# Kernel tuning notes

Measured on AMD Instinct MI355X. Metric: run time of the kernel, lower is better.

## Reference

```python
import jax, jax.numpy as jnp
import numpy as np
from jax import lax

B, C, H, W = 4, 256, 128, 128
NH = 8
HD = C // NH  # 32
K = 7         # toodd(7) -> 7
DIL = 2
NBH = K // 2  # neighborhood radius


def _window_start(i, L, k, d):
    nh = k // 2
    if d <= 1:
        return max(i - nh, 0) + (L - i - nh - 1 if i + nh >= L else 0)
    ni = i - nh * d
    if ni < 0:
        return i % d
    if i + nh * d >= L:
        imodd = i % d
        a = (L // d) * d
        b = L - a
        if imodd < b:
            return L - b + imodd - 2 * nh * d
        return a + imodd - k * d
    return ni


def _pb_start(i, L, k, d):
    nh = k // 2
    if d <= 1:
        return nh + (nh - i if i < nh else 0) + (L - i - 1 - nh if i + nh >= L else 0)
    if i - nh * d < 0:
        return k - 1 - (i // d)
    if i + nh * d >= L:
        return (L - i - 1) // d
    return nh


# [L, K] neighbor indices per axis, and [L] relative-position-bias start offsets
IDX_H = np.array([[_window_start(i, H, K, DIL) + ki * DIL for ki in range(K)] for i in range(H)], dtype=np.int32)
IDX_W = np.array([[_window_start(j, W, K, DIL) + kj * DIL for kj in range(K)] for j in range(W)], dtype=np.int32)
PB_H = np.array([_pb_start(i, H, K, DIL) for i in range(H)], dtype=np.int32)
PB_W = np.array([_pb_start(j, W, K, DIL) for j in range(W)], dtype=np.int32)


def setup_inputs() -> dict:
    key = jax.random.key(0)
    ks = jax.random.split(key, 8)
    gain = 2.0 ** (-2.5)
    x = jax.random.normal(ks[0], (B, C, H, W), jnp.float32)
    # rotary tables in [-1, 1]
    sin = jax.random.uniform(ks[1], (H, W, HD), jnp.float32, minval=-1.0, maxval=1.0)
    cos = jax.random.uniform(ks[2], (H, W, HD), jnp.float32, minval=-1.0, maxval=1.0)
    w_qkv = jax.random.normal(ks[3], (3 * C, C), jnp.float32) * gain * (2.0 / (4 * C)) ** 0.5
    b_qkv = jnp.zeros((3 * C,), jnp.float32)
    w_lepe = jax.random.normal(ks[4], (C, 1, 5, 5), jnp.float32) * 0.02
    b_lepe = jnp.zeros((C,), jnp.float32)
    w_proj = jax.random.normal(ks[5], (C, C), jnp.float32) * gain * (1.0 / C) ** 0.5
    b_proj = jnp.zeros((C,), jnp.float32)
    rpb = jax.random.normal(ks[6], (NH, 2 * K - 1, 2 * K - 1), jnp.float32) * 0.02
    return {"x": x, "sin": sin, "cos": cos, "w_qkv": w_qkv, "b_qkv": b_qkv,
            "w_lepe": w_lepe, "b_lepe": b_lepe, "w_proj": w_proj, "b_proj": b_proj, "rpb": rpb}


def _rotate_every_two(t):
    t1 = t[..., ::2]
    t2 = t[..., 1::2]
    return jnp.stack([-t2, t1], axis=-1).reshape(t.shape)


def _forward(x, sin, cos, w_qkv, b_qkv, w_lepe, b_lepe, w_proj, b_proj, rpb):
    Bx, Cx, Hx, Wx = x.shape
    # 1x1 qkv conv
    qkv = jnp.einsum('oc,bchw->bohw', w_qkv, x) + b_qkv[None, :, None, None]
    v_chan = qkv[:, 2 * Cx:]
    # LePE: depthwise 5x5 conv on v channels
    lepe = lax.conv_general_dilated(v_chan, w_lepe, (1, 1), [(2, 2), (2, 2)],
                                    feature_group_count=Cx,
                                    dimension_numbers=('NCHW', 'OIHW', 'NCHW'))
    lepe = lepe + b_lepe[None, :, None, None]

    def split_heads(t):  # [B, n*c, H, W] -> [B, n, H, W, c]
        return t.reshape(Bx, NH, HD, Hx, Wx).transpose(0, 1, 3, 4, 2)

    q = split_heads(qkv[:, :Cx])
    k = split_heads(qkv[:, Cx:2 * Cx])
    v = split_heads(v_chan)

    q = (q * cos + _rotate_every_two(q) * sin) * (HD ** -0.5)
    k = k * cos + _rotate_every_two(k) * sin

    idx_h = jnp.asarray(IDX_H)
    idx_w = jnp.asarray(IDX_W)
    pb_h = jnp.asarray(PB_H)
    pb_w = jnp.asarray(PB_W)

    # na2d_qk: dilated neighborhood scores + relative position bias
    attn_slices = []
    for ki in range(K):
        kh = jnp.take(k, idx_h[:, ki], axis=2)          # [B,n,H,W,c]
        for kj in range(K):
            khw = jnp.take(kh, idx_w[:, kj], axis=3)    # [B,n,H,W,c]
            s = jnp.einsum('bnhwc,bnhwc->bnhw', q, khw)
            bias = rpb[:, pb_h + ki][:, :, pb_w + kj]    # [n,H,W]
            attn_slices.append(s + bias[None])
    attn = jnp.stack(attn_slices, axis=-1)               # [B,n,H,W,K*K]
    attn = jax.nn.softmax(attn, axis=-1)

    # na2d_av
    out = jnp.zeros_like(v)
    idx = 0
    for ki in range(K):
        vh = jnp.take(v, idx_h[:, ki], axis=2)
        for kj in range(K):
            vhw = jnp.take(vh, idx_w[:, kj], axis=3)
            out = out + attn[..., idx, None] * vhw
            idx += 1

    out = out.transpose(0, 1, 4, 2, 3).reshape(Bx, Cx, Hx, Wx)  # merge heads
    out = out + lepe
    return jnp.einsum('oc,bchw->bohw', w_proj, out) + b_proj[None, :, None, None]


def reference(x, sin, cos, w_qkv, b_qkv, w_lepe, b_lepe, w_proj, b_proj, rpb):
    return _forward(x, sin, cos, w_qkv, b_qkv, w_lepe, b_lepe, w_proj, b_proj, rpb)
```

## Files before the change

kernel.cpp:

```cpp
#include <hip/hip_runtime.h>
#include <cstddef>

#define HW 16384
#define WID 128

typedef __attribute__((ext_vector_type(8))) short short8;
typedef __attribute__((ext_vector_type(4))) float f32x4;

__device__ __forceinline__ int wstart(int i) {
    if (i < 6) return i & 1;
    if (i >= 122) return 114 + (i & 1);
    return i - 6;
}
__device__ __forceinline__ int pbstart(int i) {
    if (i < 6) return 6 - (i >> 1);
    if (i >= 122) return (127 - i) >> 1;
    return 3;
}

__device__ __forceinline__ unsigned short bf16rne(float f) {
    unsigned u = __builtin_bit_cast(unsigned, f);
    u += 0x7FFFu + ((u >> 16) & 1u);
    return (unsigned short)(u >> 16);
}
__device__ __forceinline__ void bsplit(float f, unsigned short& h, unsigned short& l) {
    h = bf16rne(f);
    float hf = __builtin_bit_cast(float, ((unsigned)h) << 16);
    l = bf16rne(f - hf);
}

__global__ __launch_bounds__(256) void pack_t(const float* __restrict__ src, size_t bstr,
                                              unsigned short* __restrict__ dh,
                                              unsigned short* __restrict__ dl) {
    __shared__ float sm[32][260];
    const int p0 = blockIdx.x * 256, c32 = blockIdx.y, b = blockIdx.z;
    const float* s = src + (size_t)b * bstr + (size_t)(c32 * 32) * HW + p0;
    const int t = threadIdx.x;
    const int rr = t >> 3, f = t & 7;
#pragma unroll
    for (int u = 0; u < 8; u++) {
        float4 v = *(const float4*)(s + (size_t)rr * HW + (f + 8 * u) * 4);
        *(float4*)&sm[rr][(f + 8 * u) * 4] = v;
    }
    __syncthreads();
    size_t off = ((size_t)(b * 8 + c32) * HW + p0 + t) * 32;
#pragma unroll
    for (int w = 0; w < 4; w++) {
        short8 vh, vl;
#pragma unroll
        for (int e = 0; e < 8; e++) {
            unsigned short h, lo_;
            bsplit(sm[w * 8 + e][t], h, lo_);
            vh[e] = (short)h;
            vl[e] = (short)lo_;
        }
        *(short8*)&dh[off + w * 8] = vh;
        *(short8*)&dl[off + w * 8] = vl;
    }
}

template <bool QKV>
__global__ __launch_bounds__(256, 2) void gemm_mfma(
    const float* __restrict__ Wm, const unsigned short* __restrict__ xh,
    const unsigned short* __restrict__ xl, const float* __restrict__ bias,
    const float* __restrict__ sinp, const float* __restrict__ cosp,
    float* __restrict__ Y, int NMT, int MT) {
    __shared__ unsigned short As_h[128][40], As_l[128][40];
    __shared__ unsigned short Bs_h[128][40], Bs_l[128][40];
    const int bid = blockIdx.x;
    const int xcd = bid & 7, r = bid >> 3;
    const int mt = r % NMT;
    const int q2 = r / NMT;
    const int nt = xcd * 16 + (q2 & 15);
    const int b = q2 >> 4;
    const int t = threadIdx.x;
    const int lane = t & 63, wid = t >> 6;
    const int wm = wid >> 1, wn = wid & 1;
    const int m0 = mt * 128;

    f32x4 acc[4][4];
#pragma unroll
    for (int i = 0; i < 4; i++)
#pragma unroll
        for (int j = 0; j < 4; j++) acc[i][j] = (f32x4){0.f, 0.f, 0.f, 0.f};

    const int sr = t >> 1, sh = t & 1;
    const float* arow = Wm + (size_t)(m0 + sr) * 256 + sh * 16;
    const unsigned short* bh_b = xh + ((size_t)(b * 8) * HW + (size_t)nt * 128 + sr) * 32 + sh * 16;
    const unsigned short* bl_b = xl + ((size_t)(b * 8) * HW + (size_t)nt * 128 + sr) * 32 + sh * 16;

    for (int ks = 0; ks < 8; ks++) {
        {
            const float* ap = arow + ks * 32;
#pragma unroll
            for (int g = 0; g < 2; g++) {
                float4 f0 = *(const float4*)(ap + g * 8);
                float4 f1 = *(const float4*)(ap + g * 8 + 4);
                float ff[8] = {f0.x, f0.y, f0.z, f0.w, f1.x, f1.y, f1.z, f1.w};
                short8 vh, vl;
#pragma unroll
                for (int e = 0; e < 8; e++) {
                    unsigned short h, lo_;
                    bsplit(ff[e], h, lo_);
                    vh[e] = (short)h;
                    vl[e] = (short)lo_;
                }
                *(short8*)&As_h[sr][sh * 16 + g * 8] = vh;
                *(short8*)&As_l[sr][sh * 16 + g * 8] = vl;
            }
        }
        {
            const unsigned short* bp = bh_b + (size_t)ks * HW * 32;
            const unsigned short* lp = bl_b + (size_t)ks * HW * 32;
            *(short8*)&Bs_h[sr][sh * 16] = *(const short8*)(bp);
            *(short8*)&Bs_h[sr][sh * 16 + 8] = *(const short8*)(bp + 8);
            *(short8*)&Bs_l[sr][sh * 16] = *(const short8*)(lp);
            *(short8*)&Bs_l[sr][sh * 16 + 8] = *(const short8*)(lp + 8);
        }
        __syncthreads();
        const int k8 = (lane >> 4) * 8;
        short8 a_h[4], a_l[4];
#pragma unroll
        for (int mi = 0; mi < 4; mi++) {
            int am = wm * 64 + mi * 16 + (lane & 15);
            a_h[mi] = *(const short8*)&As_h[am][k8];
            a_l[mi] = *(const short8*)&As_l[am][k8];
        }
#pragma unroll
        for (int ni = 0; ni < 4; ni++) {
            int bn = wn * 64 + ni * 16 + (lane & 15);
            short8 b_h = *(const short8*)&Bs_h[bn][k8];
            short8 b_l = *(const short8*)&Bs_l[bn][k8];
#pragma unroll
            for (int mi = 0; mi < 4; mi++) {
                acc[mi][ni] = __builtin_amdgcn_mfma_f32_16x16x32_bf16(a_h[mi], b_h, acc[mi][ni], 0, 0, 0);
                acc[mi][ni] = __builtin_amdgcn_mfma_f32_16x16x32_bf16(a_h[mi], b_l, acc[mi][ni], 0, 0, 0);
                acc[mi][ni] = __builtin_amdgcn_mfma_f32_16x16x32_bf16(a_l[mi], b_h, acc[mi][ni], 0, 0, 0);
            }
        }
        __syncthreads();
    }

    const int col = lane & 15, rq = (lane >> 4) * 4;
    const int s = QKV ? (mt >> 1) : 3;
#pragma unroll
    for (int mi = 0; mi < 4; mi++) {
        int mrow = m0 + wm * 64 + mi * 16 + rq;
        float b0 = bias[mrow], b1 = bias[mrow + 1], b2 = bias[mrow + 2], b3 = bias[mrow + 3];
#pragma unroll
        for (int ni = 0; ni < 4; ni++) {
            int p = nt * 128 + wn * 64 + ni * 16 + col;
            float v0 = acc[mi][ni][0] + b0, v1 = acc[mi][ni][1] + b1;
            float v2 = acc[mi][ni][2] + b2, v3 = acc[mi][ni][3] + b3;
            if (QKV && s < 2) {
                int d0 = (mi & 1) * 16 + rq;
                const float* cp = cosp + (size_t)p * 32 + d0;
                const float* sp = sinp + (size_t)p * 32 + d0;
                float c0 = cp[0], c1 = cp[1], c2 = cp[2], c3 = cp[3];
                float s0 = sp[0], s1 = sp[1], s2 = sp[2], s3 = sp[3];
                float n0 = v0 * c0 - v1 * s0, n1 = v1 * c1 + v0 * s1;
                float n2 = v2 * c2 - v3 * s2, n3 = v3 * c3 + v2 * s3;
                if (s == 0) {
                    const float sc = 0.17677669529663687f;
                    n0 *= sc; n1 *= sc; n2 *= sc; n3 *= sc;
                }
                v0 = n0; v1 = n1; v2 = n2; v3 = n3;
            }
            float* yp = Y + ((size_t)b * MT + mrow) * HW + p;
            yp[0] = v0;
            yp[HW] = v1;
            yp[2 * HW] = v2;
            yp[3 * HW] = v3;
        }
    }
}

__global__ __launch_bounds__(256) void attn_k(const float* __restrict__ qkv,
                                              const float* __restrict__ rpb,
                                              const float* __restrict__ wl,
                                              const float* __restrict__ bl,
                                              float* __restrict__ out) {
    __shared__ float sm[14 * 128];
    const int t = threadIdx.x;
    const int ty = t >> 7;
    const int j = t & 127;
    const int i0 = blockIdx.x * 2;
    const int i = i0 + ty;
    const int n = blockIdx.y, b = blockIdx.z;
    const int r0 = wstart(i0);

    const float* qb = qkv + ((size_t)b * 768 + n * 32) * HW;
    const float* kb = qb + (size_t)256 * HW;
    const float* vb = qb + (size_t)512 * HW;
    const int p = i * WID + j;

    const int ws_ = wstart(j);
    const int ph = pbstart(i), pw = pbstart(j);

    float sc[49];
    const float* rp = rpb + n * 169;
#pragma unroll
    for (int ki = 0; ki < 7; ki++)
#pragma unroll
        for (int kj = 0; kj < 7; kj++)
            sc[ki * 7 + kj] = rp[(ph + ki) * 13 + (pw + kj)];

    const float* smb = sm + ty * 128 + ws_;

    for (int c = 0; c < 32; c++) {
        __syncthreads();
        {
            const float* plane = kb + (size_t)c * HW + r0 * WID;
#pragma unroll
            for (int u = 0; u < 7; u++) sm[t + u * 256] = plane[t + u * 256];
        }
        __syncthreads();
        float qc = qb[(size_t)c * HW + p];
#pragma unroll
        for (int ki = 0; ki < 7; ki++) {
            const float* kib = smb + ki * 256;
#pragma unroll
            for (int kj = 0; kj < 7; kj++)
                sc[ki * 7 + kj] = fmaf(qc, kib[kj * 2], sc[ki * 7 + kj]);
        }
    }

    float mx = sc[0];
#pragma unroll
    for (int u = 1; u < 49; u++) mx = fmaxf(mx, sc[u]);
    float sum = 0.0f;
#pragma unroll
    for (int u = 0; u < 49; u++) {
        sc[u] = __expf(sc[u] - mx);
        sum += sc[u];
    }
    float inv = 1.0f / sum;
#pragma unroll
    for (int u = 0; u < 49; u++) sc[u] *= inv;

    float* ob = out + ((size_t)b * 768 + n * 32) * HW + p;
    const float* wbase = wl + (size_t)(n * 32) * 25;
    const float* blb = bl + n * 32;
    for (int c = 0; c < 32; c++) {
        __syncthreads();
        {
            const float* plane = vb + (size_t)c * HW + r0 * WID;
#pragma unroll
            for (int u = 0; u < 7; u++) sm[t + u * 256] = plane[t + u * 256];
        }
        __syncthreads();
        float oc = 0.0f;
#pragma unroll
        for (int ki = 0; ki < 7; ki++) {
            const float* kib = smb + ki * 256;
#pragma unroll
            for (int kj = 0; kj < 7; kj++)
                oc = fmaf(sc[ki * 7 + kj], kib[kj * 2], oc);
        }
        const float* wrow = wbase + c * 25;
        float lac = blb[c];
#pragma unroll
        for (int di = 0; di < 5; di++) {
            int ii = i + di - 2;
            if ((unsigned)ii < 128u) {
                const float* srow = sm + (ii - r0) * 128;
                const float* wr = wrow + di * 5;
#pragma unroll
                for (int dj = 0; dj < 5; dj++) {
                    int jj = j + dj - 2;
                    if ((unsigned)jj < 128u)
                        lac = fmaf(wr[dj], srow[jj], lac);
                }
            }
        }
        ob[(size_t)c * HW] = oc + lac;
    }
}

extern "C" void kernel_launch(void* const* d_in, const int* in_sizes, int n_in,
                              void* d_out, int out_size, void* d_ws, size_t ws_size,
                              hipStream_t stream) {
    const float* x = (const float*)d_in[0];
    const float* sinp = (const float*)d_in[1];
    const float* cosp = (const float*)d_in[2];
    const float* w_qkv = (const float*)d_in[3];
    const float* b_qkv = (const float*)d_in[4];
    const float* w_lepe = (const float*)d_in[5];
    const float* b_lepe = (const float*)d_in[6];
    const float* w_proj = (const float*)d_in[7];
    const float* b_proj = (const float*)d_in[8];
    const float* rpb = (const float*)d_in[9];
    float* out = (float*)d_out;

    unsigned short* xph = (unsigned short*)d_ws;
    unsigned short* xpl = xph + 16777216ull;
    float* qkvb = (float*)(xph + 33554432ull);

    pack_t<<<dim3(64, 8, 4), 256, 0, stream>>>(x, (size_t)256 * HW, xph, xpl);
    gemm_mfma<true><<<dim3(3072), 256, 0, stream>>>(w_qkv, xph, xpl, b_qkv, sinp, cosp,
                                                    qkvb, 6, 768);
    attn_k<<<dim3(64, 8, 4), 256, 0, stream>>>(qkvb, rpb, w_lepe, b_lepe, qkvb);
    pack_t<<<dim3(64, 8, 4), 256, 0, stream>>>(qkvb, (size_t)768 * HW, xph, xpl);
    gemm_mfma<false><<<dim3(1024), 256, 0, stream>>>(w_proj, xph, xpl, b_proj, nullptr, nullptr,
                                                     out, 2, 256);
}
```

Measured before the change: 440.0 us.

## Prefetch K/V planes into registers and enlarge attention blocks to four rows

The attention kernel now processes four output rows per 512-thread block instead of two, loading a 16-row shared window per channel, which cuts redundant halo reloads. The next channel's K/V plane and q value are prefetched into registers while the current channel is computed, hiding global load latency behind the neighborhood FMAs. The grid is also flattened and remapped so that adjacent row tiles of the same batch and head land on the same XCD, for better L2 locality. The costs are higher register pressure from the prefetch buffers and larger blocks, which may lower occupancy.

```diff
diff --git a/kernel.cpp b/kernel.cpp
--- a/kernel.cpp
+++ b/kernel.cpp
@@ -175,18 +175,22 @@
     }
 }
 
-__global__ __launch_bounds__(256) void attn_k(const float* __restrict__ qkv,
+__global__ __launch_bounds__(512) void attn_k(const float* __restrict__ qkv,
                                               const float* __restrict__ rpb,
                                               const float* __restrict__ wl,
                                               const float* __restrict__ bl,
                                               float* __restrict__ out) {
-    __shared__ float sm[14 * 128];
+    __shared__ float sm[16 * 128];
     const int t = threadIdx.x;
     const int ty = t >> 7;
     const int j = t & 127;
-    const int i0 = blockIdx.x * 2;
+    const int bid = blockIdx.x;
+    const int xcd = bid & 7, rr = bid >> 3;
+    const int it = xcd * 4 + (rr & 3);
+    const int nb = rr >> 2;
+    const int n = nb & 7, b = nb >> 3;
+    const int i0 = it * 4;
     const int i = i0 + ty;
-    const int n = blockIdx.y, b = blockIdx.z;
     const int r0 = wstart(i0);
 
     const float* qb = qkv + ((size_t)b * 768 + n * 32) * HW;
@@ -194,8 +198,16 @@
     const float* vb = qb + (size_t)512 * HW;
     const int p = i * WID + j;
 
-    const int ws_ = wstart(j);
+    const int hs = wstart(i), ws_ = wstart(j);
     const int ph = pbstart(i), pw = pbstart(j);
+
+    int gofs[4];
+#pragma unroll
+    for (int s = 0; s < 4; s++) {
+        int g = r0 + ty + 4 * s;
+        if (g > 127) g = 127;
+        gofs[s] = g * WID + j;
+    }
 
     float sc[49];
     const float* rp = rpb + n * 169;
@@ -205,17 +217,24 @@
         for (int kj = 0; kj < 7; kj++)
             sc[ki * 7 + kj] = rp[(ph + ki) * 13 + (pw + kj)];
 
-    const float* smb = sm + ty * 128 + ws_;
-
+    const float* smb = sm + (hs - r0) * WID + ws_;
+
+    float rg[4], qn;
+#pragma unroll
+    for (int s = 0; s < 4; s++) rg[s] = kb[gofs[s]];
+    qn = qb[p];
     for (int c = 0; c < 32; c++) {
         __syncthreads();
-        {
-            const float* plane = kb + (size_t)c * HW + r0 * WID;
-#pragma unroll
-            for (int u = 0; u < 7; u++) sm[t + u * 256] = plane[t + u * 256];
-        }
-        __syncthreads();
-        float qc = qb[(size_t)c * HW + p];
+#pragma unroll
+        for (int s = 0; s < 4; s++) sm[(ty + 4 * s) * WID + j] = rg[s];
+        float qc = qn;
+        if (c < 31) {
+            const float* pl = kb + (size_t)(c + 1) * HW;
+#pragma unroll
+            for (int s = 0; s < 4; s++) rg[s] = pl[gofs[s]];
+            qn = qb[(size_t)(c + 1) * HW + p];
+        }
+        __syncthreads();
 #pragma unroll
         for (int ki = 0; ki < 7; ki++) {
             const float* kib = smb + ki * 256;
@@ -224,6 +243,9 @@
                 sc[ki * 7 + kj] = fmaf(qc, kib[kj * 2], sc[ki * 7 + kj]);
         }
     }
+
+#pragma unroll
+    for (int s = 0; s < 4; s++) rg[s] = vb[gofs[s]];
 
     float mx = sc[0];
 #pragma unroll
@@ -243,10 +265,12 @@
     const float* blb = bl + n * 32;
     for (int c = 0; c < 32; c++) {
         __syncthreads();
-        {
-            const float* plane = vb + (size_t)c * HW + r0 * WID;
-#pragma unroll
-            for (int u = 0; u < 7; u++) sm[t + u * 256] = plane[t + u * 256];
+#pragma unroll
+        for (int s = 0; s < 4; s++) sm[(ty + 4 * s) * WID + j] = rg[s];
+        if (c < 31) {
+            const float* pl = vb + (size_t)(c + 1) * HW;
+#pragma unroll
+            for (int s = 0; s < 4; s++) rg[s] = pl[gofs[s]];
         }
         __syncthreads();
         float oc = 0.0f;
@@ -263,7 +287,7 @@
         for (int di = 0; di < 5; di++) {
             int ii = i + di - 2;
             if ((unsigned)ii < 128u) {
-                const float* srow = sm + (ii - r0) * 128;
+                const float* srow = sm + (ii - r0) * WID;
                 const float* wr = wrow + di * 5;
 #pragma unroll
                 for (int dj = 0; dj < 5; dj++) {
@@ -299,7 +323,7 @@
     pack_t<<<dim3(64, 8, 4), 256, 0, stream>>>(x, (size_t)256 * HW, xph, xpl);
     gemm_mfma<true><<<dim3(3072), 256, 0, stream>>>(w_qkv, xph, xpl, b_qkv, sinp, cosp,
                                                     qkvb, 6, 768);
-    attn_k<<<dim3(64, 8, 4), 256, 0, stream>>>(qkvb, rpb, w_lepe, b_lepe, qkvb);
+    attn_k<<<dim3(1024), 512, 0, stream>>>(qkvb, rpb, w_lepe, b_lepe, qkvb);
     pack_t<<<dim3(64, 8, 4), 256, 0, stream>>>(qkvb, (size_t)768 * HW, xph, xpl);
     gemm_mfma<false><<<dim3(1024), 256, 0, stream>>>(w_proj, xph, xpl, b_proj, nullptr, nullptr,
                                                      out, 2, 256);
```

New measurement: 522.1 us. 18.7% more time.

## Retile attention kernel into 4x64 tiles with double-buffered two-channel LDS staging

Applied to the files above, without the earlier changes.

The neighborhood-attention kernel now works on 4-row by 64-column pixel tiles. Each tile stages an 18x88 halo window for two channels at a time into double-buffered shared memory, and the loads go through registers so the next channel pair is prefetched while the current one is computed. This halves the number of barriers, and block IDs are remapped so that row tiles are grouped per XCD for cache locality. The cost is higher register pressure (11 prefetch registers plus 49 scores) and some redundant halo loads at tile edges.

```diff
diff --git a/kernel.cpp b/kernel.cpp
--- a/kernel.cpp
+++ b/kernel.cpp
@@ -175,27 +175,52 @@
     }
 }
 
+#define SW 88
+#define CB 1408
+#define BUF 2816
 __global__ __launch_bounds__(256) void attn_k(const float* __restrict__ qkv,
                                               const float* __restrict__ rpb,
                                               const float* __restrict__ wl,
                                               const float* __restrict__ bl,
                                               float* __restrict__ out) {
-    __shared__ float sm[14 * 128];
+    __shared__ float sm[2 * BUF];
     const int t = threadIdx.x;
-    const int ty = t >> 7;
-    const int j = t & 127;
-    const int i0 = blockIdx.x * 2;
+    const int ty = t >> 6;
+    const int lj = t & 63;
+    const int bid = blockIdx.x;
+    const int xcd = bid & 7, rr = bid >> 3;
+    const int itc = rr & 3;
+    const int jt = (rr >> 2) & 1;
+    const int nb = rr >> 3;
+    const int n = nb & 7, b = nb >> 3;
+    const int it = xcd * 4 + itc;
+    const int i0 = it * 4;
+    const int j0 = jt * 64;
     const int i = i0 + ty;
-    const int n = blockIdx.y, b = blockIdx.z;
+    const int gj = j0 + lj;
     const int r0 = wstart(i0);
+    const int wc0 = wstart(j0);
 
     const float* qb = qkv + ((size_t)b * 768 + n * 32) * HW;
     const float* kb = qb + (size_t)256 * HW;
     const float* vb = qb + (size_t)512 * HW;
-    const int p = i * WID + j;
-
-    const int ws_ = wstart(j);
-    const int ph = pbstart(i), pw = pbstart(j);
+    const int p = i * WID + gj;
+
+    const int hs = wstart(i), ws_ = wstart(gj);
+    const int ph = pbstart(i), pw = pbstart(gj);
+
+    int goff[11];
+#pragma unroll
+    for (int u = 0; u < 11; u++) {
+        int d = u * 256 + t;
+        int sel = d >= CB;
+        int ld = d - sel * CB;
+        int r = ld / SW;
+        int cc = ld - r * SW;
+        int grow = r0 + r; if (grow > 127) grow = 127;
+        int gcol = wc0 + cc; if (gcol > 127) gcol = 127;
+        goff[u] = sel * HW + grow * WID + gcol;
+    }
 
     float sc[49];
     const float* rp = rpb + n * 169;
@@ -205,24 +230,44 @@
         for (int kj = 0; kj < 7; kj++)
             sc[ki * 7 + kj] = rp[(ph + ki) * 13 + (pw + kj)];
 
-    const float* smb = sm + ty * 128 + ws_;
-
-    for (int c = 0; c < 32; c++) {
+    const int abase = (hs - r0) * SW + (ws_ - wc0);
+    const int lrow0 = i - 2 - r0;
+    const int lcol0 = gj - 2 - wc0;
+
+    float rg[11];
+#pragma unroll
+    for (int u = 0; u < 11; u++) rg[u] = kb[goff[u]];
+    float qnA = qb[p], qnB = qb[HW + p];
+#pragma unroll
+    for (int u = 0; u < 11; u++) sm[u * 256 + t] = rg[u];
+    __syncthreads();
+
+    for (int cp = 0; cp < 16; cp++) {
+        const int cur = cp & 1;
+        const float* npl = (cp < 15) ? kb + (size_t)(cp + 1) * 2 * HW : vb;
+#pragma unroll
+        for (int u = 0; u < 11; u++) rg[u] = npl[goff[u]];
+        float qA = qnA, qB = qnB;
+        if (cp < 15) {
+            qnA = qb[(size_t)(2 * cp + 2) * HW + p];
+            qnB = qb[(size_t)(2 * cp + 3) * HW + p];
+        }
+        const float* s0 = sm + cur * BUF + abase;
+        const float* s1 = s0 + CB;
+#pragma unroll
+        for (int ki = 0; ki < 7; ki++) {
+            const float* a0 = s0 + ki * (2 * SW);
+            const float* a1 = s1 + ki * (2 * SW);
+#pragma unroll
+            for (int kj = 0; kj < 7; kj++) {
+                sc[ki * 7 + kj] = fmaf(qA, a0[kj * 2], sc[ki * 7 + kj]);
+                sc[ki * 7 + kj] = fmaf(qB, a1[kj * 2], sc[ki * 7 + kj]);
+            }
+        }
+        float* dst = sm + (cur ^ 1) * BUF;
+#pragma unroll
+        for (int u = 0; u < 11; u++) dst[u * 256 + t] = rg[u];
         __syncthreads();
-        {
-            const float* plane = kb + (size_t)c * HW + r0 * WID;
-#pragma unroll
-            for (int u = 0; u < 7; u++) sm[t + u * 256] = plane[t + u * 256];
-        }
-        __syncthreads();
-        float qc = qb[(size_t)c * HW + p];
-#pragma unroll
-        for (int ki = 0; ki < 7; ki++) {
-            const float* kib = smb + ki * 256;
-#pragma unroll
-            for (int kj = 0; kj < 7; kj++)
-                sc[ki * 7 + kj] = fmaf(qc, kib[kj * 2], sc[ki * 7 + kj]);
-        }
     }
 
     float mx = sc[0];
@@ -241,39 +286,50 @@
     float* ob = out + ((size_t)b * 768 + n * 32) * HW + p;
     const float* wbase = wl + (size_t)(n * 32) * 25;
     const float* blb = bl + n * 32;
-    for (int c = 0; c < 32; c++) {
+    for (int cp = 0; cp < 16; cp++) {
+        const int cur = cp & 1;
+        if (cp < 15) {
+            const float* npl = vb + (size_t)(cp + 1) * 2 * HW;
+#pragma unroll
+            for (int u = 0; u < 11; u++) rg[u] = npl[goff[u]];
+        }
+#pragma unroll
+        for (int ch = 0; ch < 2; ch++) {
+            const int cc = 2 * cp + ch;
+            const float* sv = sm + cur * BUF + ch * CB;
+            const float* sa = sv + abase;
+            float oc = 0.0f;
+#pragma unroll
+            for (int ki = 0; ki < 7; ki++) {
+                const float* a0 = sa + ki * (2 * SW);
+#pragma unroll
+                for (int kj = 0; kj < 7; kj++)
+                    oc = fmaf(sc[ki * 7 + kj], a0[kj * 2], oc);
+            }
+            const float* wrow = wbase + cc * 25;
+            float lac = blb[cc];
+#pragma unroll
+            for (int di = 0; di < 5; di++) {
+                int ii = i + di - 2;
+                if ((unsigned)ii < 128u) {
+                    const float* srow = sv + (lrow0 + di) * SW + lcol0;
+                    const float* wr = wrow + di * 5;
+#pragma unroll
+                    for (int dj = 0; dj < 5; dj++) {
+                        int jj = gj + dj - 2;
+                        if ((unsigned)jj < 128u)
+                            lac = fmaf(wr[dj], srow[dj], lac);
+                    }
+                }
+            }
+            ob[(size_t)cc * HW] = oc + lac;
+        }
+        if (cp < 15) {
+            float* dst = sm + (cur ^ 1) * BUF;
+#pragma unroll
+            for (int u = 0; u < 11; u++) dst[u * 256 + t] = rg[u];
+        }
         __syncthreads();
-        {
-            const float* plane = vb + (size_t)c * HW + r0 * WID;
-#pragma unroll
-            for (int u = 0; u < 7; u++) sm[t + u * 256] = plane[t + u * 256];
-        }
-        __syncthreads();
-        float oc = 0.0f;
-#pragma unroll
-        for (int ki = 0; ki < 7; ki++) {
-            const float* kib = smb + ki * 256;
-#pragma unroll
-            for (int kj = 0; kj < 7; kj++)
-                oc = fmaf(sc[ki * 7 + kj], kib[kj * 2], oc);
-        }
-        const float* wrow = wbase + c * 25;
-        float lac = blb[c];
-#pragma unroll
-        for (int di = 0; di < 5; di++) {
-            int ii = i + di - 2;
-            if ((unsigned)ii < 128u) {
-                const float* srow = sm + (ii - r0) * 128;
-                const float* wr = wrow + di * 5;
-#pragma unroll
-                for (int dj = 0; dj < 5; dj++) {
-                    int jj = j + dj - 2;
-                    if ((unsigned)jj < 128u)
-                        lac = fmaf(wr[dj], srow[jj], lac);
-                }
-            }
-        }
-        ob[(size_t)c * HW] = oc + lac;
     }
 }
 
@@ -299,7 +355,7 @@
     pack_t<<<dim3(64, 8, 4), 256, 0, stream>>>(x, (size_t)256 * HW, xph, xpl);
     gemm_mfma<true><<<dim3(3072), 256, 0, stream>>>(w_qkv, xph, xpl, b_qkv, sinp, cosp,
                                                     qkvb, 6, 768);
-    attn_k<<<dim3(64, 8, 4), 256, 0, stream>>>(qkvb, rpb, w_lepe, b_lepe, qkvb);
+    attn_k<<<dim3(2048), 256, 0, stream>>>(qkvb, rpb, w_lepe, b_lepe, qkvb);
     pack_t<<<dim3(64, 8, 4), 256, 0, stream>>>(qkvb, (size_t)768 * HW, xph, xpl);
     gemm_mfma<false><<<dim3(1024), 256, 0, stream>>>(w_proj, xph, xpl, b_proj, nullptr, nullptr,
                                                      out, 2, 256);
```

Result: slower. 464.8 us (+5.6%).

## Double-buffer K/V planes in LDS with async global_load_lds prefetch

Applied to the files above, without the earlier changes.

The attention kernel now stages each channel's K (and Q) plane, then each V plane, into a double-buffered LDS region using direct global-to-LDS loads. The load for channel c+1 is issued before the compute for channel c, with manual vmcnt waits and raw barriers. The goal is to overlap global memory latency with the FMA work and to drop the register round-trip of the old loads. Q is now read from LDS too. The cost is twice the LDS per block, which may lower occupancy, and the hand-written waitcnt counts are fragile: a wrong count would read stale or incomplete data.

```diff
diff --git a/kernel.cpp b/kernel.cpp
--- a/kernel.cpp
+++ b/kernel.cpp
@@ -6,6 +6,11 @@
 
 typedef __attribute__((ext_vector_type(8))) short short8;
 typedef __attribute__((ext_vector_type(4))) float f32x4;
+
+#define GLD4(g, l)                                                        \
+    __builtin_amdgcn_global_load_lds(                                     \
+        (const __attribute__((address_space(1))) unsigned int*)(g),       \
+        (__attribute__((address_space(3))) unsigned int*)(l), 4, 0, 0)
 
 __device__ __forceinline__ int wstart(int i) {
     if (i < 6) return i & 1;
@@ -175,12 +180,13 @@
     }
 }
 
+#define CBUF 2048
 __global__ __launch_bounds__(256) void attn_k(const float* __restrict__ qkv,
                                               const float* __restrict__ rpb,
                                               const float* __restrict__ wl,
                                               const float* __restrict__ bl,
                                               float* __restrict__ out) {
-    __shared__ float sm[14 * 128];
+    __shared__ float sm[2 * CBUF];
     const int t = threadIdx.x;
     const int ty = t >> 7;
     const int j = t & 127;
@@ -188,13 +194,17 @@
     const int i = i0 + ty;
     const int n = blockIdx.y, b = blockIdx.z;
     const int r0 = wstart(i0);
+    const int w64 = (t >> 6) * 64;
 
     const float* qb = qkv + ((size_t)b * 768 + n * 32) * HW;
     const float* kb = qb + (size_t)256 * HW;
     const float* vb = qb + (size_t)512 * HW;
     const int p = i * WID + j;
-
-    const int ws_ = wstart(j);
+    const float* qrow = qb + i0 * WID;
+    const float* krow = kb + r0 * WID;
+    const float* vrow = vb + r0 * WID;
+
+    const int hs = wstart(i), ws_ = wstart(j);
     const int ph = pbstart(i), pw = pbstart(j);
 
     float sc[49];
@@ -205,17 +215,29 @@
         for (int kj = 0; kj < 7; kj++)
             sc[ki * 7 + kj] = rp[(ph + ki) * 13 + (pw + kj)];
 
-    const float* smb = sm + ty * 128 + ws_;
+    const int aoff = (hs - r0) * WID + ws_;
+
+#pragma unroll
+    for (int u = 0; u < 7; u++) GLD4(krow + u * 256 + t, &sm[u * 256 + w64]);
+    GLD4(qrow + t, &sm[1792 + w64]);
 
     for (int c = 0; c < 32; c++) {
-        __syncthreads();
-        {
-            const float* plane = kb + (size_t)c * HW + r0 * WID;
-#pragma unroll
-            for (int u = 0; u < 7; u++) sm[t + u * 256] = plane[t + u * 256];
-        }
-        __syncthreads();
-        float qc = qb[(size_t)c * HW + p];
+        float* bc = sm + (c & 1) * CBUF;
+        float* bnx = sm + ((c + 1) & 1) * CBUF;
+        if (c < 31) {
+            const float* kp = krow + (size_t)(c + 1) * HW;
+#pragma unroll
+            for (int u = 0; u < 7; u++) GLD4(kp + u * 256 + t, &bnx[u * 256 + w64]);
+            GLD4(qrow + (size_t)(c + 1) * HW + t, &bnx[1792 + w64]);
+            asm volatile("s_waitcnt vmcnt(8)" ::: "memory");
+        } else {
+#pragma unroll
+            for (int u = 0; u < 7; u++) GLD4(vrow + u * 256 + t, &bnx[u * 256 + w64]);
+            asm volatile("s_waitcnt vmcnt(7)" ::: "memory");
+        }
+        __builtin_amdgcn_s_barrier();
+        float qc = bc[1792 + t];
+        const float* smb = bc + aoff;
 #pragma unroll
         for (int ki = 0; ki < 7; ki++) {
             const float* kib = smb + ki * 256;
@@ -223,6 +245,7 @@
             for (int kj = 0; kj < 7; kj++)
                 sc[ki * 7 + kj] = fmaf(qc, kib[kj * 2], sc[ki * 7 + kj]);
         }
+        __builtin_amdgcn_s_barrier();
     }
 
     float mx = sc[0];
@@ -242,13 +265,18 @@
     const float* wbase = wl + (size_t)(n * 32) * 25;
     const float* blb = bl + n * 32;
     for (int c = 0; c < 32; c++) {
-        __syncthreads();
-        {
-            const float* plane = vb + (size_t)c * HW + r0 * WID;
-#pragma unroll
-            for (int u = 0; u < 7; u++) sm[t + u * 256] = plane[t + u * 256];
-        }
-        __syncthreads();
+        float* bc = sm + (c & 1) * CBUF;
+        float* bnx = sm + ((c + 1) & 1) * CBUF;
+        if (c < 31) {
+            const float* vp = vrow + (size_t)(c + 1) * HW;
+#pragma unroll
+            for (int u = 0; u < 7; u++) GLD4(vp + u * 256 + t, &bnx[u * 256 + w64]);
+            asm volatile("s_waitcnt vmcnt(7)" ::: "memory");
+        } else {
+            asm volatile("s_waitcnt vmcnt(0)" ::: "memory");
+        }
+        __builtin_amdgcn_s_barrier();
+        const float* smb = bc + aoff;
         float oc = 0.0f;
 #pragma unroll
         for (int ki = 0; ki < 7; ki++) {
@@ -263,7 +291,7 @@
         for (int di = 0; di < 5; di++) {
             int ii = i + di - 2;
             if ((unsigned)ii < 128u) {
-                const float* srow = sm + (ii - r0) * 128;
+                const float* srow = bc + (ii - r0) * WID;
                 const float* wr = wrow + di * 5;
 #pragma unroll
                 for (int dj = 0; dj < 5; dj++) {
@@ -274,6 +302,7 @@
             }
         }
         ob[(size_t)c * HW] = oc + lac;
+        __builtin_amdgcn_s_barrier();
     }
 }
 
```

Result: faster. 421.3 us (-4.2%).
